# Optimization experiments

Measured on AMD Instinct MI355X. Metric: run time of the kernel, lower is better.

The kernel has to match this reference:

```python
import jax, jax.numpy as jnp
import numpy as np

M = 12          # grid size (m)
BIG = 1e10      # Dijkstra initial_cost default
EPS = 1e-5      # BatchNorm eps

def _conv(x, w, stride, pad):
    return jax.lax.conv_general_dilated(x, w, (stride, stride), [(pad, pad), (pad, pad)],
                                        dimension_numbers=('NCHW', 'OIHW', 'NCHW'))

def _bn(x, g, b, m, v):
    # eval-mode batchnorm with running stats
    return (x - m[:, None, None]) * (g[:, None, None] * jax.lax.rsqrt(v[:, None, None] + EPS)) + b[:, None, None]

def _maxpool(x):
    return jax.lax.reduce_window(x, -jnp.inf, jax.lax.max, (1, 1, 3, 3), (1, 1, 2, 2),
                                 [(0, 0), (0, 0), (1, 1), (1, 1)])

def _basic_block(x, w1, g1, b1, m1, v1, w2, g2, b2, m2, v2):
    y = jax.nn.relu(_bn(_conv(x, w1, 1, 1), g1, b1, m1, v1))
    y = _bn(_conv(y, w2, 1, 1), g2, b2, m2, v2)
    return jax.nn.relu(x + y)

def _relax(dist, costs):
    # Bellman-Ford relaxation on 4-neighbor grid with vertex costs
    pad_r = jnp.full((1, M), BIG, dist.dtype)
    pad_c = jnp.full((M, 1), BIG, dist.dtype)
    up = jnp.concatenate([pad_r, dist[:-1]], 0)
    down = jnp.concatenate([dist[1:], pad_r], 0)
    left = jnp.concatenate([pad_c, dist[:, :-1]], 1)
    right = jnp.concatenate([dist[:, 1:], pad_c], 1)
    nbr = jnp.minimum(jnp.minimum(up, down), jnp.minimum(left, right))
    return jnp.minimum(dist, nbr + costs)

def _shortest_path(costs):
    # single-sample shortest path (0,0)->(M-1,M-1); returns binary path indicator [M,M]
    dist = jnp.full((M, M), BIG, costs.dtype).at[0, 0].set(costs[0, 0])
    dist = jax.lax.fori_loop(0, M * M, lambda t, d: _relax(d, costs), dist)
    offs = jnp.array([[-1, 0], [1, 0], [0, -1], [0, 1]], jnp.int32)

    def body(t, carry):
        mask, i, j = carry
        mask = mask.at[i, j].set(jnp.asarray(1.0, mask.dtype))
        ni = i + offs[:, 0]
        nj = j + offs[:, 1]
        valid = (ni >= 0) & (ni < M) & (nj >= 0) & (nj < M)
        vals = jnp.where(valid, dist[jnp.clip(ni, 0, M - 1), jnp.clip(nj, 0, M - 1)], BIG)
        k = jnp.argmin(vals)
        at_start = (i == 0) & (j == 0)
        i2 = jnp.where(at_start, i, ni[k])
        j2 = jnp.where(at_start, j, nj[k])
        return mask, i2, j2

    init = (jnp.zeros((M, M), costs.dtype), jnp.int32(M - 1), jnp.int32(M - 1))
    mask, _, _ = jax.lax.fori_loop(0, M * M, body, init)
    return mask

def setup_inputs() -> dict:
    key = jax.random.key(0)
    ks = jax.random.split(key, 4)
    x = jax.random.normal(ks[0], (128, 3, 96, 96), jnp.float32)
    conv1_w = jax.random.normal(ks[1], (64, 3, 7, 7), jnp.float32) * 0.05
    blk_w = jax.random.normal(ks[2], (4, 64, 64, 3, 3), jnp.float32) * 0.05
    fc_w = jax.random.normal(ks[3], (M * M, 64 * 24 * 24), jnp.float32) * 0.01
    return {
        'x': x,
        'conv1_w': conv1_w,
        'bn1_g': jnp.ones(64), 'bn1_b': jnp.zeros(64), 'bn1_m': jnp.zeros(64), 'bn1_v': jnp.ones(64),
        'blk_w': blk_w,
        'blk_g': jnp.ones((4, 64)), 'blk_b': jnp.zeros((4, 64)),
        'blk_m': jnp.zeros((4, 64)), 'blk_v': jnp.ones((4, 64)),
        'fc_w': fc_w, 'fc_b': jnp.zeros(M * M),
    }

def reference(x, conv1_w, bn1_g, bn1_b, bn1_m, bn1_v, blk_w, blk_g, blk_b, blk_m, blk_v, fc_w, fc_b):
    h = jax.nn.relu(_bn(_conv(x, conv1_w, 2, 3), bn1_g, bn1_b, bn1_m, bn1_v))
    h = _maxpool(h)  # [B,64,24,24]
    for blk in range(2):  # resnet18 layer1: two BasicBlocks
        a, b2 = 2 * blk, 2 * blk + 1
        h = _basic_block(h,
                         blk_w[a], blk_g[a], blk_b[a], blk_m[a], blk_v[a],
                         blk_w[b2], blk_g[b2], blk_b[b2], blk_m[b2], blk_v[b2])
    cost_vec = h.reshape(h.shape[0], -1) @ fc_w.T + fc_b  # [B, m*m]
    costs = cost_vec.reshape(-1, M, M)
    path = jax.vmap(_shortest_path)(costs)  # [B, m, m] binary
    return path
```

## Files before the change

### kernel.cpp

```cpp
#include <hip/hip_runtime.h>
#include <math.h>

#define BIGF 1e10f
#define EPSF 1e-5f

typedef _Float16 f16;
typedef f16 f16x8 __attribute__((ext_vector_type(8)));
typedef float f32x4 __attribute__((ext_vector_type(4)));

static __device__ __forceinline__ f16x8 mk8(uint a, uint b, uint c, uint d) {
    union { uint u[4]; f16x8 v; } t;
    t.u[0] = a; t.u[1] = b; t.u[2] = c; t.u[3] = d;
    return t.v;
}

__global__ __launch_bounds__(256) void prepack(
    const float* __restrict__ c1w,
    const float* __restrict__ bn1g, const float* __restrict__ bn1b,
    const float* __restrict__ bn1m, const float* __restrict__ bn1v,
    const float* __restrict__ blkw,
    const float* __restrict__ blkg, const float* __restrict__ blkb,
    const float* __restrict__ blkm, const float* __restrict__ blkv,
    f16* __restrict__ wB, f16* __restrict__ wB1,
    float* __restrict__ b3, float* __restrict__ b1)
{
    int idx = blockIdx.x * 256 + threadIdx.x;
    if (idx < 147456) {
        int pos = idx;
        int j    = pos & 7;
        int lane = (pos >> 3) & 63;
        int rest = pos >> 9;
        int kf   = rest & 1;
        int r2   = rest >> 1;
        int ntl  = r2 & 3;
        int r3   = r2 >> 2;
        int tap  = r3 % 9;
        int layer= r3 / 9;
        int ic = kf * 32 + (lane >> 4) * 8 + j;
        int oc = ntl * 16 + (lane & 15);
        float s = blkg[layer * 64 + oc] * rsqrtf(blkv[layer * 64 + oc] + EPSF);
        float wv = blkw[(((size_t)layer * 64 + oc) * 64 + ic) * 9 + tap] * s;
        f16 h = (f16)wv;
        f16 lo = (f16)(wv - (float)h);
        int low9 = pos & 511;
        wB[(size_t)rest * 1024 + low9]       = h;
        wB[(size_t)rest * 1024 + 512 + low9] = lo;
    }
    int q = idx - 147456;
    if (q >= 0 && q < 28672) {
        int j = q & 7, lane = (q >> 3) & 63, rest = q >> 9;
        int hl = rest & 1, nt = (rest >> 1) & 3, kh = rest >> 3;
        int oc = nt * 16 + (lane & 15), lgq = lane >> 4;
        float v = 0.f;
        if (lgq < 3 && j < 7) {
            float s = bn1g[oc] * rsqrtf(bn1v[oc] + EPSF);
            v = c1w[((oc * 3 + lgq) * 7 + kh) * 7 + j] * s;
        }
        f16 h = (f16)v;
        wB1[q] = hl ? (f16)(v - (float)h) : h;
    }
    int k = idx - 147456 - 28672;
    if (k >= 0 && k < 256) {
        float s = blkg[k] * rsqrtf(blkv[k] + EPSF);
        b3[k] = blkb[k] - blkm[k] * s;
    }
    int l = idx - 147456 - 28672 - 256;
    if (l >= 0 && l < 64) {
        float s = bn1g[l] * rsqrtf(bn1v[l] + EPSF);
        b1[l] = bn1b[l] - bn1m[l] * s;
    }
}

__global__ __launch_bounds__(256) void conv1_mfma(
    const float* __restrict__ x, const f16* __restrict__ wB1,
    const float* __restrict__ bias,
    f16* __restrict__ outh, f16* __restrict__ outl)
{
    __shared__ char lds[18720];
    const int g = blockIdx.x, b = blockIdx.y;
    const int tid = threadIdx.x;
    const int w = tid >> 6, l = tid & 63;
    const int l15 = l & 15, lg = l >> 4;

    for (int i = tid; i < 4680; i += 256) ((uint*)lds)[i] = 0u;
    __syncthreads();
    const int ir0 = 8 * g - 5;
    const float* xb = x + (size_t)b * 27648;
    for (int u = tid; u < 2205; u += 256) {
        int cu = 1 + (u % 49);
        int rr = (u / 49) % 15;
        int ic = u / 735;
        int ir = ir0 + rr;
        uint pk_h = 0u, pk_l = 0u;
        if ((unsigned)ir < 96u) {
            int c0i = 2 * cu - 3, c1i = 2 * cu - 2;
            const float* rowp = xb + ic * 9216 + ir * 96;
            float v0 = (c0i >= 0) ? rowp[c0i] : 0.f;
            float v1 = (c1i <= 95) ? rowp[c1i] : 0.f;
            f16 h0 = (f16)v0; f16 lo0 = (f16)(v0 - (float)h0);
            f16 h1 = (f16)v1; f16 lo1 = (f16)(v1 - (float)h1);
            union { f16 f[2]; uint u32; } ph, pl;
            ph.f[0] = h0;  ph.f[1] = h1;  pk_h = ph.u32;
            pl.f[0] = lo0; pl.f[1] = lo1; pk_l = pl.u32;
        }
        int off = ic * 3120 + rr * 208 + 4 * cu;
        *(uint*)(lds + off) = pk_h;
        *(uint*)(lds + 9360 + off) = pk_l;
    }
    __syncthreads();

    f32x4 acc[4][4];
#pragma unroll
    for (int k = 0; k < 4; ++k)
#pragma unroll
        for (int nt = 0; nt < 4; ++nt) acc[k][nt] = (f32x4){0.f, 0.f, 0.f, 0.f};

    const int icB = (lg >= 3 ? 0 : lg) * 3120;
    const char* hbase = lds + icB;
    const char* lbase = lds + 9360 + icB;
    const f16* wq = wB1 + (size_t)l * 8;

    int rowoff[4], aoff[4];
#pragma unroll
    for (int k = 0; k < 4; ++k) {
        int t = w + 4 * k;
        int tt = (t < 15) ? t : 0;
        rowoff[k] = tt / 3;
        aoff[k] = 4 * ((tt % 3) * 16 + l15);
    }

#pragma unroll 1
    for (int kh = 0; kh < 7; ++kh) {
        const f16* wk = wq + kh * 4096;
        f16x8 bq[4];
#pragma unroll
        for (int nt = 0; nt < 4; ++nt)
            bq[nt] = *(const f16x8*)(const void*)(wk + nt * 1024);
#pragma unroll
        for (int k = 0; k < 4; ++k) {
            if (w + 4 * k < 15) {
                int ro = (2 * rowoff[k] + kh) * 208 + aoff[k];
                const uint* ph = (const uint*)(hbase + ro);
                const uint* pl = (const uint*)(lbase + ro);
                f16x8 ah = mk8(ph[0], ph[1], ph[2], ph[3]);
                f16x8 al = mk8(pl[0], pl[1], pl[2], pl[3]);
#pragma unroll
                for (int nt = 0; nt < 4; ++nt) {
                    acc[k][nt] = __builtin_amdgcn_mfma_f32_16x16x32_f16(ah, bq[nt], acc[k][nt], 0, 0, 0);
                    acc[k][nt] = __builtin_amdgcn_mfma_f32_16x16x32_f16(al, bq[nt], acc[k][nt], 0, 0, 0);
                }
            }
        }
#pragma unroll
        for (int nt = 0; nt < 4; ++nt)
            bq[nt] = *(const f16x8*)(const void*)(wk + nt * 1024 + 512);
#pragma unroll
        for (int k = 0; k < 4; ++k) {
            if (w + 4 * k < 15) {
                int ro = (2 * rowoff[k] + kh) * 208 + aoff[k];
                const uint* ph = (const uint*)(hbase + ro);
                f16x8 ah = mk8(ph[0], ph[1], ph[2], ph[3]);
#pragma unroll
                for (int nt = 0; nt < 4; ++nt)
                    acc[k][nt] = __builtin_amdgcn_mfma_f32_16x16x32_f16(ah, bq[nt], acc[k][nt], 0, 0, 0);
            }
        }
    }

    __syncthreads();
    float* pbuf = (float*)(void*)lds;
#pragma unroll
    for (int og = 0; og < 4; ++og) {
        float bi = bias[og * 16 + l15];
#pragma unroll
        for (int k = 0; k < 4; ++k) {
            int t = w + 4 * k;
            if (t < 15) {
                int lr = t / 3;
                int c0 = (t % 3) * 16;
#pragma unroll
                for (int r = 0; r < 4; ++r) {
                    int col = c0 + lg * 4 + r;
                    pbuf[(lr * 48 + col) * 17 + l15] = fmaxf(acc[k][og][r] + bi, 0.f);
                }
            }
        }
        __syncthreads();
#pragma unroll
        for (int it = 0; it < 3; ++it) {
            int idx = tid + it * 256;
            int oc = idx & 15, p2 = idx >> 4;
            int pc2 = p2 % 24, pr2 = p2 / 24;
            float m = -INFINITY;
#pragma unroll
            for (int kr = 0; kr < 3; ++kr) {
                int lr = 2 * pr2 + kr;
                if (g == 0 && lr == 0) continue;
#pragma unroll
                for (int kc = 0; kc < 3; ++kc) {
                    int cc = 2 * pc2 - 1 + kc;
                    if ((unsigned)cc < 48u)
                        m = fmaxf(m, pbuf[(lr * 48 + cc) * 17 + oc]);
                }
            }
            f16 h = (f16)m;
            f16 lo = (f16)(m - (float)h);
            size_t off = (size_t)b * 36864 +
                         (size_t)((2 * g + pr2) * 24 + pc2) * 64 + og * 16 + oc;
            outh[off] = h;
            outl[off] = lo;
        }
        __syncthreads();
    }
}

template<int MODE, int OUTT>
__global__ __launch_bounds__(256) void conv3_mfma(
    const f16* __restrict__ inh, const f16* __restrict__ inl,
    const f16* __restrict__ wB,
    const float* __restrict__ bias,
    const f16* __restrict__ resh, const f16* __restrict__ resl,
    f16* __restrict__ outh, f16* __restrict__ outl)
{
    __shared__ f16 lh[10 * 26 * 64];
    __shared__ f16 ll[10 * 26 * 64];
    const int r0 = blockIdx.x * 8;
    const int b  = blockIdx.y;
    const int tid = threadIdx.x;
    const int w = tid >> 6, l = tid & 63;
    const int l15 = l & 15, lg = l >> 4;

    for (int i = tid; i < 320; i += 256) {
        int arr = i >= 160; int c2 = i - arr * 160;
        int slot = c2 & 7; int pb = c2 >> 3;
        int lr = pb >> 1; int pc = (pb & 1) ? 25 : 0;
        int pix = lr * 26 + pc;
        int off = (pix * 128 + slot * 16) ^ ((pix & 7) << 4);
        *(uint4*)((arr ? (char*)ll : (char*)lh) + off) = make_uint4(0, 0, 0, 0);
    }
#pragma unroll
    for (int i = 0; i < 15; ++i) {
        int ch = tid + i * 256;
        int arr = ch >= 1920; int c2 = ch - arr * 1920;
        int slot = c2 & 7; int pix24 = c2 >> 3;
        int lr = pix24 / 24, pc = pix24 % 24;
        int ir = r0 - 1 + lr;
        uint4 v = make_uint4(0, 0, 0, 0);
        if ((unsigned)ir < 24u) {
            const f16* src = (arr ? inl : inh) +
                (((size_t)b * 576 + ir * 24 + pc) << 6) + slot * 8;
            v = *(const uint4*)(const void*)src;
        }
        int pix = lr * 26 + pc + 1;
        int off = (pix * 128 + slot * 16) ^ ((pix & 7) << 4);
        *(uint4*)((arr ? (char*)ll : (char*)lh) + off) = v;
    }

    int pr_[3], pc_[3];
#pragma unroll
    for (int mtl = 0; mtl < 3; ++mtl) {
        int lp = (w * 3 + mtl) * 16 + l15;
        pr_[mtl] = lp / 24; pc_[mtl] = lp % 24;
    }

    f32x4 acc[3][4];
#pragma unroll
    for (int m = 0; m < 3; ++m)
#pragma unroll
        for (int n = 0; n < 4; ++n) acc[m][n] = (f32x4){0.f, 0.f, 0.f, 0.f};

    __syncthreads();

#pragma unroll 1
    for (int tap = 0; tap < 9; ++tap) {
        int dr = tap / 3, dc = tap % 3;
#pragma unroll
        for (int kf = 0; kf < 2; ++kf) {
            const f16* wb = wB + (size_t)tap * 8192 + (size_t)kf * 1024 + (size_t)l * 8;
            f16x8 bh[4], bl[4];
#pragma unroll
            for (int nt = 0; nt < 4; ++nt) {
                bh[nt] = *(const f16x8*)(const void*)(wb + nt * 2048);
                bl[nt] = *(const f16x8*)(const void*)(wb + nt * 2048 + 512);
            }
#pragma unroll
            for (int mtl = 0; mtl < 3; ++mtl) {
                int pix = (pr_[mtl] + dr) * 26 + (pc_[mtl] + dc);
                int off = (pix * 128 + kf * 64 + lg * 16) ^ ((pix & 7) << 4);
                f16x8 ah = *(const f16x8*)((const char*)lh + off);
                f16x8 al = *(const f16x8*)((const char*)ll + off);
#pragma unroll
                for (int nt = 0; nt < 4; ++nt) {
                    acc[mtl][nt] = __builtin_amdgcn_mfma_f32_16x16x32_f16(ah, bh[nt], acc[mtl][nt], 0, 0, 0);
                    acc[mtl][nt] = __builtin_amdgcn_mfma_f32_16x16x32_f16(ah, bl[nt], acc[mtl][nt], 0, 0, 0);
                    acc[mtl][nt] = __builtin_amdgcn_mfma_f32_16x16x32_f16(al, bh[nt], acc[mtl][nt], 0, 0, 0);
                }
            }
        }
    }

    float bi[4];
#pragma unroll
    for (int nt = 0; nt < 4; ++nt) bi[nt] = bias[nt * 16 + l15];

#pragma unroll
    for (int mtl = 0; mtl < 3; ++mtl) {
#pragma unroll
        for (int nt = 0; nt < 4; ++nt) {
#pragma unroll
            for (int r = 0; r < 4; ++r) {
                int lp = (w * 3 + mtl) * 16 + lg * 4 + r;
                int p = r0 * 24 + lp;
                int oc = nt * 16 + l15;
                float v = acc[mtl][nt][r] + bi[nt];
                if (MODE) {
                    size_t ridx = (size_t)b * 36864 + (size_t)p * 64 + oc;
                    v += (float)resh[ridx] + (float)resl[ridx];
                }
                v = fmaxf(v, 0.f);
                f16 h = (f16)v;
                f16 lo = (f16)(v - (float)h);
                size_t oidx = OUTT ? ((size_t)b * 36864 + (size_t)oc * 576 + p)
                                   : ((size_t)b * 36864 + (size_t)p * 64 + oc);
                outh[oidx] = h;
                outl[oidx] = lo;
            }
        }
    }
}

#define FC_KSPLIT 32

__global__ __launch_bounds__(256) void fc_mfma(
    const f16* __restrict__ Ath, const f16* __restrict__ Atl,
    const float* __restrict__ Bw, float* __restrict__ part)
{
    __shared__ f16 As[2][128 * 40];
    __shared__ f16 Bs[2][16 * 40];
    const int nt = blockIdx.x;
    const int ks = blockIdx.y;
    const int tid = threadIdx.x;
    const int w = tid >> 6, l = tid & 63;
    const int l15 = l & 15, lg = l >> 4;
    const int k0b = ks * 1152;

    f32x4 acc[2];
    acc[0] = (f32x4){0.f, 0.f, 0.f, 0.f};
    acc[1] = (f32x4){0.f, 0.f, 0.f, 0.f};

    const int bn = tid >> 4, bkl = (tid & 15) * 2;
#pragma unroll 1
    for (int st = 0; st < 36; ++st) {
        int k0 = k0b + st * 32;
        __syncthreads();
#pragma unroll
        for (int i = 0; i < 4; ++i) {
            int ch = tid + i * 256;
            int arr = ch >= 512; int c2 = ch - arr * 512;
            int m = c2 >> 2, slot = c2 & 3;
            const f16* src = (arr ? Atl : Ath) + (size_t)m * 36864 + k0 + slot * 8;
            *(uint4*)(void*)&As[arr][m * 40 + slot * 8] = *(const uint4*)(const void*)src;
        }
        {
            float2 f2 = *(const float2*)&Bw[(size_t)(nt * 16 + bn) * 36864 + k0 + bkl];
            f16 h0 = (f16)f2.x, h1 = (f16)f2.y;
            Bs[0][bn * 40 + bkl] = h0;     Bs[0][bn * 40 + bkl + 1] = h1;
            Bs[1][bn * 40 + bkl] = (f16)(f2.x - (float)h0);
            Bs[1][bn * 40 + bkl + 1] = (f16)(f2.y - (float)h1);
        }
        __syncthreads();
        f16x8 bh = *(const f16x8*)(const void*)&Bs[0][l15 * 40 + lg * 8];
        f16x8 bl = *(const f16x8*)(const void*)&Bs[1][l15 * 40 + lg * 8];
#pragma unroll
        for (int mtl = 0; mtl < 2; ++mtl) {
            int m = w * 32 + mtl * 16 + l15;
            f16x8 ah = *(const f16x8*)(const void*)&As[0][m * 40 + lg * 8];
            f16x8 al = *(const f16x8*)(const void*)&As[1][m * 40 + lg * 8];
            acc[mtl] = __builtin_amdgcn_mfma_f32_16x16x32_f16(ah, bh, acc[mtl], 0, 0, 0);
            acc[mtl] = __builtin_amdgcn_mfma_f32_16x16x32_f16(ah, bl, acc[mtl], 0, 0, 0);
            acc[mtl] = __builtin_amdgcn_mfma_f32_16x16x32_f16(al, bh, acc[mtl], 0, 0, 0);
        }
    }
#pragma unroll
    for (int mtl = 0; mtl < 2; ++mtl)
#pragma unroll
        for (int r = 0; r < 4; ++r) {
            int m = w * 32 + mtl * 16 + lg * 4 + r;
            int n = nt * 16 + l15;
            part[((size_t)ks * 128 + m) * 144 + n] = acc[mtl][r];
        }
}

__global__ __launch_bounds__(256) void fc_reduce(
    const float* __restrict__ part, const float* __restrict__ bias,
    float* __restrict__ costs)
{
    int idx = blockIdx.x * 256 + threadIdx.x;
    if (idx >= 128 * 144) return;
    float sum = bias[idx % 144];
    for (int s = 0; s < FC_KSPLIT; ++s) sum += part[(size_t)s * (128 * 144) + idx];
    costs[idx] = sum;
}

__global__ __launch_bounds__(192) void shortest_path(
    const float* __restrict__ costs, float* __restrict__ out)
{
    __shared__ float dA[144], dB[144], cs[144], mask[144];
    const int b = blockIdx.x, tid = threadIdx.x;
    if (tid < 144) {
        float c = costs[b * 144 + tid];
        cs[tid] = c;
        dA[tid] = (tid == 0) ? c : BIGF;
        mask[tid] = 0.f;
    }
    __syncthreads();
    float* cur = dA; float* nxt = dB;
    for (int it = 0; it < 144; ++it) {
        if (tid < 144) {
            int i = tid / 12, j = tid % 12;
            float up = (i > 0)  ? cur[tid - 12] : BIGF;
            float dn = (i < 11) ? cur[tid + 12] : BIGF;
            float lf = (j > 0)  ? cur[tid - 1]  : BIGF;
            float rt = (j < 11) ? cur[tid + 1]  : BIGF;
            float nb = fminf(fminf(up, dn), fminf(lf, rt));
            nxt[tid] = fminf(cur[tid], nb + cs[tid]);
        }
        __syncthreads();
        float* tp = cur; cur = nxt; nxt = tp;
    }
    if (tid == 0) {
        int i = 11, j = 11;
        const int di[4] = {-1, 1, 0, 0};
        const int dj[4] = {0, 0, -1, 1};
        for (int it = 0; it < 144; ++it) {
            mask[i * 12 + j] = 1.f;
            float vals[4];
#pragma unroll
            for (int k = 0; k < 4; ++k) {
                int ni = i + di[k], nj = j + dj[k];
                bool valid = (ni >= 0) && (ni < 12) && (nj >= 0) && (nj < 12);
                vals[k] = valid ? cur[ni * 12 + nj] : BIGF;
            }
            float best = vals[0]; int kb = 0;
#pragma unroll
            for (int k = 1; k < 4; ++k)
                if (vals[k] < best) { best = vals[k]; kb = k; }
            if (!(i == 0 && j == 0)) { i += di[kb]; j += dj[kb]; }
        }
    }
    __syncthreads();
    if (tid < 144) out[b * 144 + tid] = mask[tid];
}

extern "C" void kernel_launch(void* const* d_in, const int* in_sizes, int n_in,
                              void* d_out, int out_size, void* d_ws, size_t ws_size,
                              hipStream_t stream) {
    const float* x    = (const float*)d_in[0];
    const float* c1w  = (const float*)d_in[1];
    const float* bn1g = (const float*)d_in[2];
    const float* bn1b = (const float*)d_in[3];
    const float* bn1m = (const float*)d_in[4];
    const float* bn1v = (const float*)d_in[5];
    const float* blkw = (const float*)d_in[6];
    const float* blkg = (const float*)d_in[7];
    const float* blkb = (const float*)d_in[8];
    const float* blkm = (const float*)d_in[9];
    const float* blkv = (const float*)d_in[10];
    const float* fcw  = (const float*)d_in[11];
    const float* fcb  = (const float*)d_in[12];
    float* out = (float*)d_out;
    char* ws = (char*)d_ws;

    const size_t APL = 9437184;
    f16* a0h = (f16*)(ws);
    f16* a0l = (f16*)(ws + APL);
    f16* a1h = (f16*)(ws + 2 * APL);
    f16* a1l = (f16*)(ws + 3 * APL);
    f16* a2h = (f16*)(ws + 4 * APL);
    f16* a2l = (f16*)(ws + 5 * APL);
    float* costs = (float*)(ws + 6 * APL);
    float* part  = (float*)(ws + 6 * APL + 73728);
    f16*   wB    = (f16*)  (ws + 6 * APL + 73728 + 2359296);
    float* b3    = (float*)(ws + 6 * APL + 73728 + 2359296 + 589824);
    float* b1    = (float*)(ws + 6 * APL + 73728 + 2359296 + 589824 + 1024);
    f16*   wB1   = (f16*)  (ws + 6 * APL + 73728 + 2359296 + 589824 + 1280);

    prepack<<<dim3(690), dim3(256), 0, stream>>>(
        c1w, bn1g, bn1b, bn1m, bn1v, blkw, blkg, blkb, blkm, blkv,
        wB, wB1, b3, b1);

    conv1_mfma<<<dim3(12, 128), dim3(256), 0, stream>>>(x, wB1, b1, a0h, a0l);

    conv3_mfma<0, 0><<<dim3(3, 128), dim3(256), 0, stream>>>(
        a0h, a0l, wB + 0 * 73728, b3 + 0,   nullptr, nullptr, a1h, a1l);
    conv3_mfma<1, 0><<<dim3(3, 128), dim3(256), 0, stream>>>(
        a1h, a1l, wB + 1 * 73728, b3 + 64,  a0h, a0l, a2h, a2l);
    conv3_mfma<0, 0><<<dim3(3, 128), dim3(256), 0, stream>>>(
        a2h, a2l, wB + 2 * 73728, b3 + 128, nullptr, nullptr, a1h, a1l);
    conv3_mfma<1, 1><<<dim3(3, 128), dim3(256), 0, stream>>>(
        a1h, a1l, wB + 3 * 73728, b3 + 192, a2h, a2l, a0h, a0l);

    fc_mfma<<<dim3(9, FC_KSPLIT), dim3(256), 0, stream>>>(a0h, a0l, fcw, part);
    fc_reduce<<<dim3(72), dim3(256), 0, stream>>>(part, fcb, costs);
    shortest_path<<<dim3(128), dim3(192), 0, stream>>>(costs, out);
}
```

Before: 242.2 us.

## Run shortest-path relaxation in registers with wave shuffles instead of barriers

```diff
diff --git a/kernel.cpp b/kernel.cpp
--- a/kernel.cpp
+++ b/kernel.cpp
@@ -402,54 +402,88 @@
     costs[idx] = sum;
 }
 
-__global__ __launch_bounds__(192) void shortest_path(
+__global__ __launch_bounds__(64) void shortest_path(
     const float* __restrict__ costs, float* __restrict__ out)
 {
-    __shared__ float dA[144], dB[144], cs[144], mask[144];
-    const int b = blockIdx.x, tid = threadIdx.x;
-    if (tid < 144) {
-        float c = costs[b * 144 + tid];
-        cs[tid] = c;
-        dA[tid] = (tid == 0) ? c : BIGF;
-        mask[tid] = 0.f;
+    __shared__ float dls[4][144];
+    __shared__ float msk[4][144];
+    const int tid = threadIdx.x;
+    const int grp = tid >> 4, li = tid & 15;
+    const int s = blockIdx.x * 4 + grp;
+    const bool act = li < 12;
+
+    float c[12], d[12];
+#pragma unroll
+    for (int j = 0; j < 12; ++j) { c[j] = BIGF; d[j] = BIGF; }
+    if (act) {
+#pragma unroll
+        for (int j = 0; j < 12; ++j) c[j] = costs[s * 144 + li * 12 + j];
+    }
+    if (li == 0) d[0] = c[0];
+
+    for (int i = tid; i < 576; i += 64) ((float*)msk)[i] = 0.f;
+
+#pragma unroll 1
+    for (int it = 0; it < 144; ++it) {
+        float up[12], dn[12];
+#pragma unroll
+        for (int j = 0; j < 12; ++j) {
+            up[j] = __shfl_up(d[j], 1, 16);
+            dn[j] = __shfl_down(d[j], 1, 16);
+        }
+        float nd[12];
+#pragma unroll
+        for (int j = 0; j < 12; ++j) {
+            float u  = (li > 0)  ? up[j] : BIGF;
+            float dd = (li < 11) ? dn[j] : BIGF;
+            float lf = (j > 0)   ? d[j - 1] : BIGF;
+            float rt = (j < 11)  ? d[j + 1] : BIGF;
+            float nb = fminf(fminf(u, dd), fminf(lf, rt));
+            nd[j] = fminf(d[j], nb + c[j]);
+        }
+#pragma unroll
+        for (int j = 0; j < 12; ++j) d[j] = nd[j];
+    }
+
+    if (act) {
+#pragma unroll
+        for (int j = 0; j < 12; ++j) dls[grp][li * 12 + j] = d[j];
     }
     __syncthreads();
-    float* cur = dA; float* nxt = dB;
+
+    bool done = (li != 0);
+    int pi = 11, pj = 11;
+#pragma unroll 1
     for (int it = 0; it < 144; ++it) {
-        if (tid < 144) {
-            int i = tid / 12, j = tid % 12;
-            float up = (i > 0)  ? cur[tid - 12] : BIGF;
-            float dn = (i < 11) ? cur[tid + 12] : BIGF;
-            float lf = (j > 0)  ? cur[tid - 1]  : BIGF;
-            float rt = (j < 11) ? cur[tid + 1]  : BIGF;
-            float nb = fminf(fminf(up, dn), fminf(lf, rt));
-            nxt[tid] = fminf(cur[tid], nb + cs[tid]);
-        }
-        __syncthreads();
-        float* tp = cur; cur = nxt; nxt = tp;
-    }
-    if (tid == 0) {
-        int i = 11, j = 11;
-        const int di[4] = {-1, 1, 0, 0};
-        const int dj[4] = {0, 0, -1, 1};
-        for (int it = 0; it < 144; ++it) {
-            mask[i * 12 + j] = 1.f;
-            float vals[4];
-#pragma unroll
-            for (int k = 0; k < 4; ++k) {
-                int ni = i + di[k], nj = j + dj[k];
-                bool valid = (ni >= 0) && (ni < 12) && (nj >= 0) && (nj < 12);
-                vals[k] = valid ? cur[ni * 12 + nj] : BIGF;
-            }
-            float best = vals[0]; int kb = 0;
-#pragma unroll
-            for (int k = 1; k < 4; ++k)
-                if (vals[k] < best) { best = vals[k]; kb = k; }
-            if (!(i == 0 && j == 0)) { i += di[kb]; j += dj[kb]; }
-        }
+        if (!done) {
+            msk[grp][pi * 12 + pj] = 1.f;
+            if (pi == 0 && pj == 0) {
+                done = true;
+            } else {
+                const int di[4] = {-1, 1, 0, 0};
+                const int dj[4] = {0, 0, -1, 1};
+                float vals[4];
+#pragma unroll
+                for (int k = 0; k < 4; ++k) {
+                    int ni = pi + di[k], nj = pj + dj[k];
+                    bool valid = (ni >= 0) && (ni < 12) && (nj >= 0) && (nj < 12);
+                    vals[k] = valid ? dls[grp][ni * 12 + nj] : BIGF;
+                }
+                float best = vals[0]; int kb = 0;
+#pragma unroll
+                for (int k = 1; k < 4; ++k)
+                    if (vals[k] < best) { best = vals[k]; kb = k; }
+                pi += di[kb]; pj += dj[kb];
+            }
+        }
+        if (__all(done)) break;
     }
     __syncthreads();
-    if (tid < 144) out[b * 144 + tid] = mask[tid];
+
+    if (act) {
+#pragma unroll
+        for (int j = 0; j < 12; ++j) out[s * 144 + li * 12 + j] = msk[grp][li * 12 + j];
+    }
 }
 
 extern "C" void kernel_launch(void* const* d_in, const int* in_sizes, int n_in,
@@ -502,5 +536,5 @@
 
     fc_mfma<<<dim3(9, FC_KSPLIT), dim3(256), 0, stream>>>(a0h, a0l, fcw, part);
     fc_reduce<<<dim3(72), dim3(256), 0, stream>>>(part, fcb, costs);
-    shortest_path<<<dim3(128), dim3(192), 0, stream>>>(costs, out);
-}
+    shortest_path<<<dim3(32), dim3(64), 0, stream>>>(costs, out);
+}
```

Result: slower. 282.5 us (+16.6%).
